# Kernel optimization log

Hardware: AMD Instinct MI355X
Metric: run time of the kernel (lower is better)

Reference implementation:

```python
import jax, jax.numpy as jnp
import numpy as np

B, S, D, H = 4, 2048, 1024, 16
DK = D // H


def setup_inputs() -> dict:
    key = jax.random.key(0)
    ks = jax.random.split(key, 10)
    std = 0.02
    inp = {
        "input": jax.random.normal(ks[0], (B, S, D), dtype=jnp.float32),
        "attention_reweight": jax.random.uniform(ks[1], (B, S), dtype=jnp.float32),
        "mask": 1,
        "Wq": jax.random.normal(ks[2], (D, D), dtype=jnp.float32) * std,
        "bq": jnp.zeros((D,), dtype=jnp.float32),
        "Wk": jax.random.normal(ks[3], (D, D), dtype=jnp.float32) * std,
        "bk": jnp.zeros((D,), dtype=jnp.float32),
        "Wv": jax.random.normal(ks[4], (D, D), dtype=jnp.float32) * std,
        "bv": jnp.zeros((D,), dtype=jnp.float32),
        "Wo": jax.random.normal(ks[5], (D, D), dtype=jnp.float32) * std,
        "bo": jnp.zeros((D,), dtype=jnp.float32),
    }
    return inp


def reference(input, attention_reweight, mask, Wq, bq, Wk, bk, Wv, bv, Wo, bo):
    b, s, d = input.shape
    # QKV projections (torch Linear: x @ W.T + b)
    q = (input @ Wq.T + bq).reshape(b, s, H, DK).transpose(0, 2, 1, 3)  # [B,H,S,dk]
    k = (input @ Wk.T + bk).reshape(b, s, H, DK).transpose(0, 2, 1, 3)
    v = (input @ Wv.T + bv).reshape(b, s, H, DK).transpose(0, 2, 1, 3)

    scores = jnp.einsum("bhqd,bhkd->bhqk", q, k)  # [B,H,S,S]
    if mask:
        causal = jnp.triu(jnp.ones((s, s), dtype=scores.dtype), k=1)
        scores = scores - causal * 1e9
    scores = scores / jnp.sqrt(jnp.asarray(DK, dtype=jnp.float32))
    # reweight per key position: [B,S] broadcast over heads and query positions
    scores = scores * attention_reweight[:, None, None, :]

    attn = jax.nn.softmax(scores, axis=-1)
    out = jnp.einsum("bhqk,bhkd->bhqd", attn, v)  # [B,H,S,dk]
    out = out.transpose(0, 2, 1, 3).reshape(b, s, d)
    return out @ Wo.T + bo
```

## Files before the change

### kernel.cpp

```cpp
#include <hip/hip_runtime.h>
#include <math.h>

#define B_  4
#define S_  2048
#define D_  1024
#define H_  16
#define DK_ 64

typedef __bf16 bf16x8 __attribute__((ext_vector_type(8)));
typedef float  f32x4  __attribute__((ext_vector_type(4)));

__device__ __forceinline__ unsigned short f2bf(float f) {
  unsigned int u = __builtin_bit_cast(unsigned int, f);
  u += 0x7fffu + ((u >> 16) & 1u);
  return (unsigned short)(u >> 16);
}

__device__ __forceinline__ unsigned short bfbits(float f) {
  __bf16 h = (__bf16)f;
  return __builtin_bit_cast(unsigned short, h);
}

__device__ __forceinline__ f32x4 mfma16(bf16x8 a, bf16x8 b, f32x4 c) {
  return __builtin_amdgcn_mfma_f32_16x16x32_bf16(a, b, c, 0, 0, 0);
}

__device__ __forceinline__ void gl_lds16(const unsigned short* g, unsigned short* l) {
  __builtin_amdgcn_global_load_lds(
      (const __attribute__((address_space(1))) void*)g,
      (__attribute__((address_space(3))) void*)l, 16, 0, 0);
}

__global__ void SAA_cast_bf16(const float* __restrict__ src,
                              unsigned short* __restrict__ dst, int n4) {
  int i = blockIdx.x * blockDim.x + threadIdx.x;
  int stride = gridDim.x * blockDim.x;
  for (; i < n4; i += stride) {
    float4 v = reinterpret_cast<const float4*>(src)[i];
    ushort4 o;
    o.x = f2bf(v.x); o.y = f2bf(v.y); o.z = f2bf(v.z); o.w = f2bf(v.w);
    reinterpret_cast<ushort4*>(dst)[i] = o;
  }
}

__global__ void SAA_cast4(const float* __restrict__ s0, const float* __restrict__ s1,
                          const float* __restrict__ s2, const float* __restrict__ s3,
                          unsigned short* __restrict__ d0, unsigned short* __restrict__ d1,
                          unsigned short* __restrict__ d2, unsigned short* __restrict__ d3,
                          int n4) {
  const float* src = (blockIdx.y == 0) ? s0 : (blockIdx.y == 1) ? s1
                   : (blockIdx.y == 2) ? s2 : s3;
  unsigned short* dst = (blockIdx.y == 0) ? d0 : (blockIdx.y == 1) ? d1
                      : (blockIdx.y == 2) ? d2 : d3;
  int i = blockIdx.x * blockDim.x + threadIdx.x;
  int stride = gridDim.x * blockDim.x;
  for (; i < n4; i += stride) {
    float4 v = reinterpret_cast<const float4*>(src)[i];
    ushort4 o;
    o.x = f2bf(v.x); o.y = f2bf(v.y); o.z = f2bf(v.z); o.w = f2bf(v.w);
    reinterpret_cast<ushort4*>(dst)[i] = o;
  }
}

__global__ __launch_bounds__(512)
void SAA_gemm_qkv(const unsigned short* __restrict__ Xb,
                  const unsigned short* __restrict__ Wqb,
                  const unsigned short* __restrict__ Wkb,
                  const unsigned short* __restrict__ Wvb,
                  const float* __restrict__ bq,
                  const float* __restrict__ bk,
                  const float* __restrict__ bv,
                  const float* __restrict__ rw,
                  unsigned short* __restrict__ Qo,
                  unsigned short* __restrict__ Ko,
                  unsigned short* __restrict__ Vto)
{
  const int K = D_;
  __shared__ __attribute__((aligned(16))) unsigned short sA[2][128 * 64];
  __shared__ __attribute__((aligned(16))) unsigned short sB[2][3][128 * 64];

  const int t = threadIdx.x;
  const int w = t >> 6, l = t & 63;
  const int wm = w >> 1, wn = w & 1;
  const int lr = l & 15, lg = l >> 4;
  const int r7 = lr & 7;

  const int m0 = blockIdx.y * 128;
  const int n0 = blockIdx.x * 128;

  const unsigned short* gA = Xb + (size_t)m0 * K;
  const unsigned short* gB0 = Wqb + (size_t)n0 * K;
  const unsigned short* gB1 = Wkb + (size_t)n0 * K;
  const unsigned short* gB2 = Wvb + (size_t)n0 * K;

  int srow[2], soff[2];
#pragma unroll
  for (int i = 0; i < 2; i++) {
    const int c = i * 512 + t;
    srow[i] = c >> 3;
    soff[i] = ((c & 7) ^ (srow[i] & 7)) * 8;
  }

#define STAGE(s, k0)                                                          \
  do {                                                                        \
    _Pragma("unroll")                                                         \
    for (int i = 0; i < 2; i++) {                                             \
      const size_t go = (size_t)srow[i] * K + (k0) + soff[i];                 \
      const int dl = (i * 512 + t) * 8;                                       \
      gl_lds16(gA  + go, &sA[s][dl]);                                         \
      gl_lds16(gB0 + go, &sB[s][0][dl]);                                      \
      gl_lds16(gB1 + go, &sB[s][1][dl]);                                      \
      gl_lds16(gB2 + go, &sB[s][2][dl]);                                      \
    }                                                                         \
  } while (0)

  STAGE(0, 0);

  f32x4 acc[3][2][4] = {};

#pragma unroll 2
  for (int T = 0; T < 16; ++T) {
    __syncthreads();
    if (T + 1 < 16) STAGE((T + 1) & 1, (T + 1) * 64);

    const unsigned short* At = sA[T & 1];
#pragma unroll
    for (int ks = 0; ks < 2; ++ks) {
      const int swk = (((ks * 4 + lg) ^ r7) << 3);
      bf16x8 afr[2];
#pragma unroll
      for (int mi = 0; mi < 2; ++mi)
        afr[mi] = *reinterpret_cast<const bf16x8*>(
            &At[(wm * 32 + mi * 16 + lr) * 64 + swk]);
#pragma unroll
      for (int mat = 0; mat < 3; ++mat) {
        const unsigned short* Bt = sB[T & 1][mat];
        bf16x8 bfr[4];
#pragma unroll
        for (int n = 0; n < 4; ++n)
          bfr[n] = *reinterpret_cast<const bf16x8*>(
              &Bt[(wn * 64 + n * 16 + lr) * 64 + swk]);
#pragma unroll
        for (int mi = 0; mi < 2; ++mi)
#pragma unroll
          for (int n = 0; n < 4; ++n)
            acc[mat][mi][n] = mfma16(afr[mi], bfr[n], acc[mat][mi][n]);
      }
    }
  }
#undef STAGE

#pragma unroll
  for (int n = 0; n < 4; ++n) {
    const int col = n0 + wn * 64 + n * 16 + lr;
    const int h = col >> 6, dk = col & 63;
    const float bqv = bq[col], bkv = bk[col], bvv = bv[col];
#pragma unroll
    for (int mi = 0; mi < 2; ++mi) {
#pragma unroll
      for (int r = 0; r < 4; ++r) {
        const int row = m0 + wm * 32 + mi * 16 + lg * 4 + r;
        const int b = row >> 11, s = row & 2047;
        Qo[(((size_t)b * H_ + h) * S_ + s) * DK_ + dk] = bfbits(acc[0][mi][n][r] + bqv);
        Ko[(((size_t)b * H_ + h) * S_ + s) * DK_ + dk] =
            bfbits((acc[1][mi][n][r] + bkv) * (0.18033688011112042f * rw[row]));
        Vto[(((size_t)b * H_ + h) * DK_ + dk) * S_ + s] = bfbits(acc[2][mi][n][r] + bvv);
      }
    }
  }
}

__global__ __launch_bounds__(512)
void SAA_attn(const unsigned short* __restrict__ Q,
              const unsigned short* __restrict__ Kb,
              const unsigned short* __restrict__ Vt,
              const int* __restrict__ maskp,
              unsigned short* __restrict__ Cb)
{
  const int pairid = blockIdx.x;
  const int h = blockIdx.y, b = blockIdx.z;
  const int t = threadIdx.x, w = t >> 6, l = t & 63;
  const int lr = l & 15, lg = l >> 4;
  const int mask = maskp[0];

  __shared__ __attribute__((aligned(16))) unsigned short Kt[2][64 * 64];
  __shared__ __attribute__((aligned(16))) unsigned short Vl[2][64 * 64];
  __shared__ __attribute__((aligned(16))) unsigned short Pl[8][16 * 64];

  const size_t bh = (size_t)b * H_ + h;
  const unsigned short* Qbh = Q + bh * S_ * DK_;
  const unsigned short* Kbh = Kb + bh * S_ * DK_;
  const unsigned short* Vbh = Vt + bh * DK_ * S_;
  unsigned short* Pw = &Pl[w][0];

  const int r0 = t >> 3, cc0 = t & 7;
  const int sw0 = (cc0 ^ (r0 & 7)) * 8;

  for (int half = 0; half < 2; ++half) {
    const int qb = half ? (15 - pairid) : pairid;
    const int q0 = qb * 128;
    const int wq = q0 + w * 16;

    bf16x8 qf[2];
#pragma unroll
    for (int ks = 0; ks < 2; ks++)
      qf[ks] = *reinterpret_cast<const bf16x8*>(
          &Qbh[(size_t)(wq + lr) * DK_ + ks * 32 + lg * 8]);

    f32x4 acc[4] = {};
    float lrun[4] = {0.f, 0.f, 0.f, 0.f};

    const int nkt = mask ? (qb * 2 + 2) : (S_ / 64);
    const int wqmax = wq + 15;

    __syncthreads();

    gl_lds16(Kbh + (size_t)r0 * DK_ + sw0, &Kt[0][t * 8]);
    gl_lds16(Vbh + (size_t)r0 * S_ + sw0,  &Vl[0][t * 8]);
    int cur = 0;

    for (int kt = 0; kt < nkt; ++kt) {
      __syncthreads();
      if (kt + 1 < nkt) {
        const int kn = (kt + 1) * 64;
        const int nb = cur ^ 1;
        gl_lds16(Kbh + (size_t)(kn + r0) * DK_ + sw0, &Kt[nb][t * 8]);
        gl_lds16(Vbh + (size_t)r0 * S_ + kn + sw0,    &Vl[nb][t * 8]);
      }

      const int k0 = kt * 64;
      const bool active = (!mask) || (k0 <= wqmax);
      if (active) {
        const unsigned short* Kc = &Kt[cur][0];
        const unsigned short* Vc = &Vl[cur][0];

        f32x4 sc[4] = {};
#pragma unroll
        for (int ks = 0; ks < 2; ++ks) {
          const int swk = (((ks * 4 + lg) ^ (lr & 7)) << 3);
#pragma unroll
          for (int t2 = 0; t2 < 4; ++t2) {
            bf16x8 kf = *reinterpret_cast<const bf16x8*>(&Kc[(t2 * 16 + lr) * 64 + swk]);
            sc[t2] = mfma16(qf[ks], kf, sc[t2]);
          }
        }

        const bool needmask = mask && (k0 + 63 > wq);

#pragma unroll
        for (int r = 0; r < 4; r++) {
          const int row = wq + lg * 4 + r;
          float v0 = sc[0][r], v1 = sc[1][r];
          float v2 = sc[2][r], v3 = sc[3][r];
          if (needmask) {
            if (k0 + lr      > row) v0 = -1e30f;
            if (k0 + 16 + lr > row) v1 = -1e30f;
            if (k0 + 32 + lr > row) v2 = -1e30f;
            if (k0 + 48 + lr > row) v3 = -1e30f;
          }
          const float p0 = __builtin_amdgcn_exp2f(v0);
          const float p1 = __builtin_amdgcn_exp2f(v1);
          const float p2 = __builtin_amdgcn_exp2f(v2);
          const float p3 = __builtin_amdgcn_exp2f(v3);
          lrun[r] += (p0 + p1) + (p2 + p3);
          const int prow = lg * 4 + r;
          const int pr7 = prow & 7;
          const int pbase = prow * 64 + (lr & 7);
          const int hi = lr >> 3;
          Pw[pbase + (((0 + hi) ^ pr7) << 3)] = bfbits(p0);
          Pw[pbase + (((2 + hi) ^ pr7) << 3)] = bfbits(p1);
          Pw[pbase + (((4 + hi) ^ pr7) << 3)] = bfbits(p2);
          Pw[pbase + (((6 + hi) ^ pr7) << 3)] = bfbits(p3);
        }

#pragma unroll
        for (int ks = 0; ks < 2; ++ks) {
          const int swk = (((ks * 4 + lg) ^ (lr & 7)) << 3);
          bf16x8 pf = *reinterpret_cast<const bf16x8*>(&Pw[lr * 64 + swk]);
#pragma unroll
          for (int dt = 0; dt < 4; ++dt) {
            bf16x8 vf = *reinterpret_cast<const bf16x8*>(&Vc[(dt * 16 + lr) * 64 + swk]);
            acc[dt] = mfma16(pf, vf, acc[dt]);
          }
        }
      }
      cur ^= 1;
    }

#pragma unroll
    for (int r = 0; r < 4; r++) {
      float rs = lrun[r];
      rs += __shfl_xor(rs, 1);
      rs += __shfl_xor(rs, 2);
      rs += __shfl_xor(rs, 4);
      rs += __shfl_xor(rs, 8);
      lrun[r] = __builtin_amdgcn_rcpf(rs);
    }
#pragma unroll
    for (int dt = 0; dt < 4; dt++) {
#pragma unroll
      for (int r = 0; r < 4; r++) {
        const int row = wq + lg * 4 + r;
        const int col = h * DK_ + dt * 16 + lr;
        Cb[((size_t)b * S_ + row) * D_ + col] = bfbits(acc[dt][r] * lrun[r]);
      }
    }
  }
}

__global__ __launch_bounds__(256)
void SAA_gemm_out(const unsigned short* __restrict__ Cb,
                  const unsigned short* __restrict__ Wob,
                  const float* __restrict__ bo,
                  float* __restrict__ Y)
{
  const int K = D_;
  __shared__ __attribute__((aligned(16))) unsigned short lA[2][128 * 64];
  __shared__ __attribute__((aligned(16))) unsigned short lB[2][128 * 64];

  const int t = threadIdx.x;
  const int w = t >> 6, l = t & 63;
  const int wr = w >> 1, wc = w & 1;
  const int lr = l & 15, lg = l >> 4;
  const int r7 = lr & 7;

  const int m0 = blockIdx.y * 128;
  const int n0 = blockIdx.x * 128;

  const unsigned short* gA = Cb + (size_t)m0 * K;
  const unsigned short* gB = Wob + (size_t)n0 * K;

  int srow[4], soff[4];
#pragma unroll
  for (int i = 0; i < 4; i++) {
    const int c = i * 256 + t;
    srow[i] = c >> 3;
    soff[i] = ((c & 7) ^ (srow[i] & 7)) * 8;
  }

#define STAGEO(s, k0)                                                         \
  do {                                                                        \
    _Pragma("unroll")                                                         \
    for (int i = 0; i < 4; i++) {                                             \
      const size_t go = (size_t)srow[i] * K + (k0) + soff[i];                 \
      const int dl = (i * 256 + t) * 8;                                       \
      gl_lds16(gA + go, &lA[s][dl]);                                          \
      gl_lds16(gB + go, &lB[s][dl]);                                          \
    }                                                                         \
  } while (0)

  STAGEO(0, 0);

  f32x4 acc[4][4] = {};

#pragma unroll 2
  for (int T = 0; T < 16; ++T) {
    __syncthreads();
    if (T + 1 < 16) STAGEO((T + 1) & 1, (T + 1) * 64);

    const unsigned short* At = lA[T & 1];
    const unsigned short* Bt = lB[T & 1];
#pragma unroll
    for (int ks = 0; ks < 2; ks++) {
      const int swk = (((ks * 4 + lg) ^ r7) << 3);
      bf16x8 af[4], bfr[4];
#pragma unroll
      for (int i = 0; i < 4; i++)
        af[i] = *reinterpret_cast<const bf16x8*>(&At[(wr * 64 + i * 16 + lr) * 64 + swk]);
#pragma unroll
      for (int j = 0; j < 4; j++)
        bfr[j] = *reinterpret_cast<const bf16x8*>(&Bt[(wc * 64 + j * 16 + lr) * 64 + swk]);
#pragma unroll
      for (int i = 0; i < 4; i++)
#pragma unroll
        for (int j = 0; j < 4; j++)
          acc[i][j] = mfma16(af[i], bfr[j], acc[i][j]);
    }
  }
#undef STAGEO

#pragma unroll
  for (int j = 0; j < 4; j++) {
    const int col = n0 + wc * 64 + j * 16 + lr;
    const float bsv = bo[col];
#pragma unroll
    for (int i = 0; i < 4; i++) {
#pragma unroll
      for (int r = 0; r < 4; r++) {
        const int row = m0 + wr * 64 + i * 16 + lg * 4 + r;
        Y[(size_t)row * D_ + col] = acc[i][j][r] + bsv;
      }
    }
  }
}

extern "C" void kernel_launch(void* const* d_in, const int* in_sizes, int n_in,
                              void* d_out, int out_size, void* d_ws, size_t ws_size,
                              hipStream_t stream) {
  const float* input = (const float*)d_in[0];
  const float* rw    = (const float*)d_in[1];
  const int*   maskp = (const int*)d_in[2];
  const float* Wq = (const float*)d_in[3];
  const float* bq = (const float*)d_in[4];
  const float* Wk = (const float*)d_in[5];
  const float* bk = (const float*)d_in[6];
  const float* Wv = (const float*)d_in[7];
  const float* bv = (const float*)d_in[8];
  const float* Wo = (const float*)d_in[9];
  const float* bo = (const float*)d_in[10];

  char* ws = (char*)d_ws;
  unsigned short* Xb  = (unsigned short*)(ws);
  unsigned short* Wqb = (unsigned short*)(ws + (16u << 20));
  unsigned short* Wkb = (unsigned short*)(ws + (18u << 20));
  unsigned short* Wvb = (unsigned short*)(ws + (20u << 20));
  unsigned short* Wob = (unsigned short*)(ws + (22u << 20));
  unsigned short* Qo  = (unsigned short*)(ws + (24u << 20));
  unsigned short* Ko  = (unsigned short*)(ws + (40u << 20));
  unsigned short* Vto = (unsigned short*)(ws + (56u << 20));
  unsigned short* Cb  = Xb;

  SAA_cast_bf16<<<2048, 256, 0, stream>>>(input, Xb, (B_ * S_ * D_) / 4);
  SAA_cast4<<<dim3(512, 4), 256, 0, stream>>>(Wq, Wk, Wv, Wo, Wqb, Wkb, Wvb, Wob,
                                              (D_ * D_) / 4);

  SAA_gemm_qkv<<<dim3(8, 64), 512, 0, stream>>>(Xb, Wqb, Wkb, Wvb, bq, bk, bv, rw,
                                                Qo, Ko, Vto);
  SAA_attn<<<dim3(8, 16, 4), 512, 0, stream>>>(Qo, Ko, Vto, maskp, Cb);
  SAA_gemm_out<<<dim3(8, 64), 256, 0, stream>>>(Cb, Wob, bo, (float*)d_out);
}
```

Baseline: 182.4 us.

## Give each attention wave two 16-row query tiles, halving threads per block

```diff
diff --git a/kernel.cpp b/kernel.cpp
--- a/kernel.cpp
+++ b/kernel.cpp
@@ -88,7 +88,7 @@
   const int m0 = blockIdx.y * 128;
   const int n0 = blockIdx.x * 128;
 
-  const unsigned short* gA = Xb + (size_t)m0 * K;
+  const unsigned short* gA  = Xb  + (size_t)m0 * K;
   const unsigned short* gB0 = Wqb + (size_t)n0 * K;
   const unsigned short* gB1 = Wkb + (size_t)n0 * K;
   const unsigned short* gB2 = Wvb + (size_t)n0 * K;
@@ -170,7 +170,7 @@
   }
 }
 
-__global__ __launch_bounds__(512)
+__global__ __launch_bounds__(256)
 void SAA_attn(const unsigned short* __restrict__ Q,
               const unsigned short* __restrict__ Kb,
               const unsigned short* __restrict__ Vt,
@@ -185,7 +185,7 @@
 
   __shared__ __attribute__((aligned(16))) unsigned short Kt[2][64 * 64];
   __shared__ __attribute__((aligned(16))) unsigned short Vl[2][64 * 64];
-  __shared__ __attribute__((aligned(16))) unsigned short Pl[8][16 * 64];
+  __shared__ __attribute__((aligned(16))) unsigned short Pl[4][32 * 64];
 
   const size_t bh = (size_t)b * H_ + h;
   const unsigned short* Qbh = Q + bh * S_ * DK_;
@@ -193,30 +193,34 @@
   const unsigned short* Vbh = Vt + bh * DK_ * S_;
   unsigned short* Pw = &Pl[w][0];
 
-  const int r0 = t >> 3, cc0 = t & 7;
-  const int sw0 = (cc0 ^ (r0 & 7)) * 8;
+  const int r0 = t >> 3;
+  const int sw0 = (((t & 7) ^ (r0 & 7)) * 8);
 
   for (int half = 0; half < 2; ++half) {
     const int qb = half ? (15 - pairid) : pairid;
     const int q0 = qb * 128;
-    const int wq = q0 + w * 16;
-
-    bf16x8 qf[2];
-#pragma unroll
-    for (int ks = 0; ks < 2; ks++)
-      qf[ks] = *reinterpret_cast<const bf16x8*>(
-          &Qbh[(size_t)(wq + lr) * DK_ + ks * 32 + lg * 8]);
-
-    f32x4 acc[4] = {};
-    float lrun[4] = {0.f, 0.f, 0.f, 0.f};
+    const int wq = q0 + w * 32;
+
+    bf16x8 qf[2][2];
+#pragma unroll
+    for (int m = 0; m < 2; ++m)
+#pragma unroll
+      for (int ks = 0; ks < 2; ++ks)
+        qf[m][ks] = *reinterpret_cast<const bf16x8*>(
+            &Qbh[(size_t)(wq + m * 16 + lr) * DK_ + ks * 32 + lg * 8]);
+
+    f32x4 acc[2][4] = {};
+    float lrun[2][4] = {};
 
     const int nkt = mask ? (qb * 2 + 2) : (S_ / 64);
-    const int wqmax = wq + 15;
+    const int wqmax = wq + 31;
 
     __syncthreads();
 
-    gl_lds16(Kbh + (size_t)r0 * DK_ + sw0, &Kt[0][t * 8]);
-    gl_lds16(Vbh + (size_t)r0 * S_ + sw0,  &Vl[0][t * 8]);
+    gl_lds16(Kbh + (size_t)r0 * DK_ + sw0,        &Kt[0][t * 8]);
+    gl_lds16(Kbh + (size_t)(r0 + 32) * DK_ + sw0, &Kt[0][2048 + t * 8]);
+    gl_lds16(Vbh + (size_t)r0 * S_ + sw0,         &Vl[0][t * 8]);
+    gl_lds16(Vbh + (size_t)(r0 + 32) * S_ + sw0,  &Vl[0][2048 + t * 8]);
     int cur = 0;
 
     for (int kt = 0; kt < nkt; ++kt) {
@@ -224,8 +228,10 @@
       if (kt + 1 < nkt) {
         const int kn = (kt + 1) * 64;
         const int nb = cur ^ 1;
-        gl_lds16(Kbh + (size_t)(kn + r0) * DK_ + sw0, &Kt[nb][t * 8]);
-        gl_lds16(Vbh + (size_t)r0 * S_ + kn + sw0,    &Vl[nb][t * 8]);
+        gl_lds16(Kbh + (size_t)(kn + r0) * DK_ + sw0,      &Kt[nb][t * 8]);
+        gl_lds16(Kbh + (size_t)(kn + r0 + 32) * DK_ + sw0, &Kt[nb][2048 + t * 8]);
+        gl_lds16(Vbh + (size_t)r0 * S_ + kn + sw0,         &Vl[nb][t * 8]);
+        gl_lds16(Vbh + (size_t)(r0 + 32) * S_ + kn + sw0,  &Vl[nb][2048 + t * 8]);
       }
 
       const int k0 = kt * 64;
@@ -234,53 +240,59 @@
         const unsigned short* Kc = &Kt[cur][0];
         const unsigned short* Vc = &Vl[cur][0];
 
-        f32x4 sc[4] = {};
+        f32x4 sc[2][4] = {};
 #pragma unroll
         for (int ks = 0; ks < 2; ++ks) {
           const int swk = (((ks * 4 + lg) ^ (lr & 7)) << 3);
 #pragma unroll
           for (int t2 = 0; t2 < 4; ++t2) {
             bf16x8 kf = *reinterpret_cast<const bf16x8*>(&Kc[(t2 * 16 + lr) * 64 + swk]);
-            sc[t2] = mfma16(qf[ks], kf, sc[t2]);
+            sc[0][t2] = mfma16(qf[0][ks], kf, sc[0][t2]);
+            sc[1][t2] = mfma16(qf[1][ks], kf, sc[1][t2]);
           }
         }
 
         const bool needmask = mask && (k0 + 63 > wq);
 
 #pragma unroll
-        for (int r = 0; r < 4; r++) {
-          const int row = wq + lg * 4 + r;
-          float v0 = sc[0][r], v1 = sc[1][r];
-          float v2 = sc[2][r], v3 = sc[3][r];
-          if (needmask) {
-            if (k0 + lr      > row) v0 = -1e30f;
-            if (k0 + 16 + lr > row) v1 = -1e30f;
-            if (k0 + 32 + lr > row) v2 = -1e30f;
-            if (k0 + 48 + lr > row) v3 = -1e30f;
+        for (int m = 0; m < 2; ++m) {
+#pragma unroll
+          for (int r = 0; r < 4; ++r) {
+            const int row = wq + m * 16 + lg * 4 + r;
+            float v0 = sc[m][0][r], v1 = sc[m][1][r];
+            float v2 = sc[m][2][r], v3 = sc[m][3][r];
+            if (needmask) {
+              if (k0 + lr      > row) v0 = -1e30f;
+              if (k0 + 16 + lr > row) v1 = -1e30f;
+              if (k0 + 32 + lr > row) v2 = -1e30f;
+              if (k0 + 48 + lr > row) v3 = -1e30f;
+            }
+            const float p0 = __builtin_amdgcn_exp2f(v0);
+            const float p1 = __builtin_amdgcn_exp2f(v1);
+            const float p2 = __builtin_amdgcn_exp2f(v2);
+            const float p3 = __builtin_amdgcn_exp2f(v3);
+            lrun[m][r] += (p0 + p1) + (p2 + p3);
+            const int prow = m * 16 + lg * 4 + r;
+            const int pr7 = prow & 7;
+            const int pbase = prow * 64 + (lr & 7);
+            const int hi = lr >> 3;
+            Pw[pbase + (((0 + hi) ^ pr7) << 3)] = bfbits(p0);
+            Pw[pbase + (((2 + hi) ^ pr7) << 3)] = bfbits(p1);
+            Pw[pbase + (((4 + hi) ^ pr7) << 3)] = bfbits(p2);
+            Pw[pbase + (((6 + hi) ^ pr7) << 3)] = bfbits(p3);
           }
-          const float p0 = __builtin_amdgcn_exp2f(v0);
-          const float p1 = __builtin_amdgcn_exp2f(v1);
-          const float p2 = __builtin_amdgcn_exp2f(v2);
-          const float p3 = __builtin_amdgcn_exp2f(v3);
-          lrun[r] += (p0 + p1) + (p2 + p3);
-          const int prow = lg * 4 + r;
-          const int pr7 = prow & 7;
-          const int pbase = prow * 64 + (lr & 7);
-          const int hi = lr >> 3;
-          Pw[pbase + (((0 + hi) ^ pr7) << 3)] = bfbits(p0);
-          Pw[pbase + (((2 + hi) ^ pr7) << 3)] = bfbits(p1);
-          Pw[pbase + (((4 + hi) ^ pr7) << 3)] = bfbits(p2);
-          Pw[pbase + (((6 + hi) ^ pr7) << 3)] = bfbits(p3);
         }
 
 #pragma unroll
         for (int ks = 0; ks < 2; ++ks) {
           const int swk = (((ks * 4 + lg) ^ (lr & 7)) << 3);
-          bf16x8 pf = *reinterpret_cast<const bf16x8*>(&Pw[lr * 64 + swk]);
+          bf16x8 pf0 = *reinterpret_cast<const bf16x8*>(&Pw[lr * 64 + swk]);
+          bf16x8 pf1 = *reinterpret_cast<const bf16x8*>(&Pw[(16 + lr) * 64 + swk]);
 #pragma unroll
           for (int dt = 0; dt < 4; ++dt) {
             bf16x8 vf = *reinterpret_cast<const bf16x8*>(&Vc[(dt * 16 + lr) * 64 + swk]);
-            acc[dt] = mfma16(pf, vf, acc[dt]);
+            acc[0][dt] = mfma16(pf0, vf, acc[0][dt]);
+            acc[1][dt] = mfma16(pf1, vf, acc[1][dt]);
           }
         }
       }
@@ -288,21 +300,27 @@
     }
 
 #pragma unroll
-    for (int r = 0; r < 4; r++) {
-      float rs = lrun[r];
-      rs += __shfl_xor(rs, 1);
-      rs += __shfl_xor(rs, 2);
-      rs += __shfl_xor(rs, 4);
-      rs += __shfl_xor(rs, 8);
-      lrun[r] = __builtin_amdgcn_rcpf(rs);
-    }
-#pragma unroll
-    for (int dt = 0; dt < 4; dt++) {
-#pragma unroll
-      for (int r = 0; r < 4; r++) {
-        const int row = wq + lg * 4 + r;
-        const int col = h * DK_ + dt * 16 + lr;
-        Cb[((size_t)b * S_ + row) * D_ + col] = bfbits(acc[dt][r] * lrun[r]);
+    for (int m = 0; m < 2; ++m) {
+#pragma unroll
+      for (int r = 0; r < 4; ++r) {
+        float rs = lrun[m][r];
+        rs += __shfl_xor(rs, 1);
+        rs += __shfl_xor(rs, 2);
+        rs += __shfl_xor(rs, 4);
+        rs += __shfl_xor(rs, 8);
+        lrun[m][r] = __builtin_amdgcn_rcpf(rs);
+      }
+    }
+#pragma unroll
+    for (int m = 0; m < 2; ++m) {
+#pragma unroll
+      for (int dt = 0; dt < 4; ++dt) {
+#pragma unroll
+        for (int r = 0; r < 4; ++r) {
+          const int row = wq + m * 16 + lg * 4 + r;
+          const int col = h * DK_ + dt * 16 + lr;
+          Cb[((size_t)b * S_ + row) * D_ + col] = bfbits(acc[m][dt][r] * lrun[m][r]);
+        }
       }
     }
   }
@@ -426,6 +444,6 @@
 
   SAA_gemm_qkv<<<dim3(8, 64), 512, 0, stream>>>(Xb, Wqb, Wkb, Wvb, bq, bk, bv, rw,
                                                 Qo, Ko, Vto);
-  SAA_attn<<<dim3(8, 16, 4), 512, 0, stream>>>(Qo, Ko, Vto, maskp, Cb);
+  SAA_attn<<<dim3(8, 16, 4), 256, 0, stream>>>(Qo, Ko, Vto, maskp, Cb);
   SAA_gemm_out<<<dim3(8, 64), 256, 0, stream>>>(Cb, Wob, bo, (float*)d_out);
 }
```

Result: slower. 194.1 us (+6.4%).
